# Kernel tuning notes

Hardware: AMD Instinct MI355X
Metric: run time of the kernel (lower is better)

The kernel has to match this reference:

```python
import jax, jax.numpy as jnp
import numpy as np

VOCAB = 512
EMB = 256
HID = 64
T_HORIZON = 0.05


def setup_inputs() -> dict:
    key = jax.random.key(0)
    ks = jax.random.split(key, 6)
    B, L = 32, 4096
    x = jax.random.randint(ks[0], (B, L), 0, VOCAB, dtype=jnp.int64 if jax.config.jax_enable_x64 else jnp.int32)
    emb_table = jax.random.normal(ks[1], (VOCAB, EMB), dtype=jnp.float32)
    W1 = jax.random.normal(ks[2], (EMB, HID), dtype=jnp.float32) * (1.0 / np.sqrt(EMB))
    b1 = jnp.zeros((HID,), dtype=jnp.float32)
    W2 = jax.random.normal(ks[3], (HID, VOCAB), dtype=jnp.float32) * (1.0 / np.sqrt(HID))
    b2 = jnp.full((VOCAB,), 0.1, dtype=jnp.float32)  # torch: bias.data.fill_(0.1)
    return {"x": x, "emb_table": emb_table, "W1": W1, "b1": b1, "W2": W2, "b2": b2, "steps": 5}


def reference(x, emb_table, W1, b1, W2, b2, steps):
    """Vectorized Gillespie-style Markov jump simulation.

    Equivalent to the torch loop: intensity is computed once per step from the
    current state, then every (b, l) position samples a candidate next state
    from softmax(intensity) with the self-transition zeroed and renormalized
    (== categorical over logits with the current state masked to -inf), and
    accepts it with prob 1 - exp(-rate * dt).
    """
    V = emb_table.shape[0]
    dt = T_HORIZON / steps
    key = jax.random.key(42)
    keys = jax.random.split(key, steps)
    vocab_ids = jnp.arange(V)

    def step(x_t, k):
        # intensity: [B, L, V]
        h = jax.nn.relu(emb_table[x_t] @ W1 + b1)
        intensity = h @ W2 + b2
        # mask self-transition (softmax * (1 - onehot) then renormalize)
        self_mask = x_t[..., None] == vocab_ids  # [B, L, V] bool
        masked_logits = jnp.where(self_mask, -jnp.inf, intensity)
        k1, k2 = jax.random.split(k)
        next_state = jax.random.categorical(k1, masked_logits)  # [B, L]
        rate = jnp.take_along_axis(intensity, next_state[..., None], axis=-1)[..., 0]
        accept_prob = 1.0 - jnp.exp(-rate * dt)
        u = jax.random.uniform(k2, x_t.shape, dtype=rate.dtype)
        x_t = jnp.where(u < accept_prob, next_state.astype(x_t.dtype), x_t)
        return x_t, None

    x_final, _ = jax.lax.scan(step, x, keys)
    return x_final
```

## Files before the change

kernel.cpp:

```cpp
#include <hip/hip_runtime.h>
#include <stdint.h>


#define VOCAB  512
#define EMB    256
#define HID    64
#define NPOS   (32 * 4096)
#define STEPS  5
#define JWAVES 8192

__host__ __device__ __forceinline__ void tf2x32(uint32_t k0, uint32_t k1,
                                                uint32_t x0, uint32_t x1,
                                                uint32_t& o0, uint32_t& o1) {
  uint32_t ks2 = k0 ^ k1 ^ 0x1BD11BDAu;
  x0 += k0; x1 += k1;
#define TFR(r) { x0 += x1; x1 = (x1 << (r)) | (x1 >> (32 - (r))); x1 ^= x0; }
  TFR(13) TFR(15) TFR(26) TFR(6)
  x0 += k1;  x1 += ks2 + 1u;
  TFR(17) TFR(29) TFR(16) TFR(24)
  x0 += ks2; x1 += k0 + 2u;
  TFR(13) TFR(15) TFR(26) TFR(6)
  x0 += k0;  x1 += k1 + 3u;
  TFR(17) TFR(29) TFR(16) TFR(24)
  x0 += k1;  x1 += ks2 + 4u;
  TFR(13) TFR(15) TFR(26) TFR(6)
  x0 += ks2; x1 += k0 + 5u;
#undef TFR
  o0 = x0; o1 = x1;
}

struct Keys {
  uint32_t k1a[STEPS], k1b[STEPS];
  uint32_t k2a[STEPS], k2b[STEPS];
};

__global__ __launch_bounds__(512)
void build_table(const float* __restrict__ emb,
                 const float* __restrict__ W1,
                 const float* __restrict__ b1,
                 const float* __restrict__ W2,
                 const float* __restrict__ b2,
                 float* __restrict__ I,
                 float* __restrict__ P,
                 float* __restrict__ pthr,
                 uint32_t* __restrict__ counter) {
  const int s   = blockIdx.x;
  const int tid = threadIdx.x;
  if (s == 0 && tid == 0) *counter = 0u;

  __shared__ double part[8][HID];
  __shared__ double hd[HID];
  __shared__ float  redmax[8];

  const int hid = tid & (HID - 1);
  const int kq  = tid >> 6;
  const float* e = emb + s * EMB;
  double acc = 0.0;
#pragma unroll
  for (int ib = 0; ib < 32; ib += 16) {
    float ev[16], wv[16];
#pragma unroll
    for (int i = 0; i < 16; ++i) {
      const int k = kq + 8 * (ib + i);
      ev[i] = e[k];
      wv[i] = W1[k * HID + hid];
    }
#pragma unroll
    for (int i = 0; i < 16; ++i)
      acc += (double)ev[i] * (double)wv[i];
  }
  part[kq][hid] = acc;
  __syncthreads();
  if (kq == 0) {
    const double a = ((part[0][hid] + part[1][hid]) + (part[2][hid] + part[3][hid]))
                   + ((part[4][hid] + part[5][hid]) + (part[6][hid] + part[7][hid]));
    const float m = (float)a + b1[hid];
    hd[hid] = (double)(m > 0.0f ? m : 0.0f);
  }
  __syncthreads();

  double acc2 = 0.0;
#pragma unroll
  for (int kb = 0; kb < HID; kb += 16) {
    float wv[16];
#pragma unroll
    for (int i = 0; i < 16; ++i)
      wv[i] = W2[(kb + i) * VOCAB + tid];
#pragma unroll
    for (int i = 0; i < 16; ++i)
      acc2 += hd[kb + i] * (double)wv[i];
  }
  const float val = (float)acc2 + b2[tid];
  I[s * VOCAB + tid] = val;
  const float z = (-val) * 0.01f;
  const float pv = 1.0f - (float)exp((double)z);
  P[s * VOCAB + tid] = pv;

  float lmax = pv;
  for (int off = 32; off > 0; off >>= 1)
    lmax = fmaxf(lmax, __shfl_xor(lmax, off, 64));
  if ((tid & 63) == 0) redmax[tid >> 6] = lmax;
  __syncthreads();
  if (tid == 0) {
    float m = redmax[0];
#pragma unroll
    for (int i = 1; i < 8; ++i) m = fmaxf(m, redmax[i]);
    pthr[s] = m;
  }
}

__global__ __launch_bounds__(256)
void screen_kernel(const int* __restrict__ x_in,
                   const float* __restrict__ pthr,
                   int* __restrict__ x_out,
                   uint32_t* __restrict__ counter,
                   uint32_t* __restrict__ list,
                   Keys K) {
  const int pos = blockIdx.x * 256 + threadIdx.x;
  const int s = x_in[pos];
  const float th = pthr[s];
  int mask = 0;
#pragma unroll
  for (int t = 0; t < STEPS; ++t) {
    uint32_t w0, w1;
    tf2x32(K.k2a[t], K.k2b[t], 0u, (uint32_t)pos, w0, w1);
    const float u = __uint_as_float((((w0 ^ w1) >> 9) | 0x3f800000u)) - 1.0f;
    if (u < th) mask |= (1 << t);
  }
  x_out[pos] = s;

  const int lane = threadIdx.x & 63, wv = threadIdx.x >> 6;
  const unsigned long long bal = __ballot(mask != 0);
  __shared__ uint32_t wcnt[4], wbase[4];
  if (lane == 0) wcnt[wv] = (uint32_t)__popcll(bal);
  __syncthreads();
  if (threadIdx.x == 0) {
    const uint32_t tot = wcnt[0] + wcnt[1] + wcnt[2] + wcnt[3];
    uint32_t b = atomicAdd(counter, tot);
    wbase[0] = b; b += wcnt[0];
    wbase[1] = b; b += wcnt[1];
    wbase[2] = b; b += wcnt[2];
    wbase[3] = b;
  }
  __syncthreads();
  if (mask) {
    const uint32_t off = wbase[wv] +
        (uint32_t)__popcll(bal & ((1ull << lane) - 1ull));
    list[off] = (uint32_t)pos | ((uint32_t)mask << 20);
  }
}

__global__ __launch_bounds__(128)
void jump_kernel(const int* __restrict__ x_in,
                 const float* __restrict__ I,
                 const float* __restrict__ P,
                 const float* __restrict__ pthr,
                 int* __restrict__ x_out,
                 const uint32_t* __restrict__ counter,
                 const uint32_t* __restrict__ list,
                 Keys K) {
  const int lane = threadIdx.x & 63;
  const int wid  = (blockIdx.x << 1) | (threadIdx.x >> 6);
  const int n = (int)*counter;
  const float TINYF = 1.17549435e-38f;
  const float NEGINF = -__builtin_inff();

  for (int i = wid; i < n; i += JWAVES) {
    const uint32_t e = list[i];
    const int pos = (int)(e & 0xFFFFFu);
    int m = (int)(e >> 20);
    int s = __builtin_amdgcn_readfirstlane(x_in[pos]);

    while (m) {
      const int t = __builtin_ctz(m);
      m &= m - 1;

      uint32_t a0, a1;
      tf2x32(K.k2a[t], K.k2b[t], 0u, (uint32_t)pos, a0, a1);
      const float u = __uint_as_float((((a0 ^ a1) >> 9) | 0x3f800000u)) - 1.0f;

      const float* row = I + s * VOCAB;
      float rv[8];
#pragma unroll
      for (int j = 0; j < 8; ++j)
        rv[j] = row[lane + (j << 6)];

      const uint32_t fbase = ((uint32_t)pos << 9) + (uint32_t)lane;
      uint32_t bits[8];
#pragma unroll
      for (int j = 0; j < 8; ++j) {
        uint32_t w0, w1;
        tf2x32(K.k1a[t], K.k1b[t], 0u, fbase + ((uint32_t)j << 6), w0, w1);
        bits[j] = w0 ^ w1;
      }

      float valC[8];
      float bestC = NEGINF;
#pragma unroll
      for (int j = 0; j < 8; ++j) {
        float ufv = __uint_as_float((bits[j] >> 9) | 0x3f800000u) - 1.0f;
        if (ufv == 0.0f) ufv = TINYF;
        const float gC = -__logf(-__logf(ufv));
        const int v = lane + (j << 6);
        valC[j] = (v == s) ? NEGINF : rv[j] + gC;
        bestC = fmaxf(bestC, valC[j]);
      }
      for (int off = 32; off > 0; off >>= 1)
        bestC = fmaxf(bestC, __shfl_xor(bestC, off, 64));
      const float thresh = bestC - 0.015625f;

      float best = NEGINF;
      int bidx = 0x7FFFFFFF;
#pragma unroll
      for (int j = 0; j < 8; ++j) {
        if (valC[j] >= thresh) {
          float ufv = __uint_as_float((bits[j] >> 9) | 0x3f800000u) - 1.0f;
          if (ufv == 0.0f) ufv = TINYF;
          const float g = -logf(-logf(ufv));
          const float val = rv[j] + g;
          const int v = lane + (j << 6);
          if (val > best) { best = val; bidx = v; }
        }
      }
      for (int off = 32; off > 0; off >>= 1) {
        const float ob = __shfl_xor(best, off, 64);
        const int   oi = __shfl_xor(bidx, off, 64);
        if (ob > best || (ob == best && oi < bidx)) { best = ob; bidx = oi; }
      }
      bidx = __builtin_amdgcn_readfirstlane(bidx);

      const float pacc = P[s * VOCAB + bidx];
      if (u < pacc) {
        s = bidx;
        const float th2 = pthr[s];
        int m2 = 0;
        for (int t2 = t + 1; t2 < STEPS; ++t2) {
          uint32_t w0, w1;
          tf2x32(K.k2a[t2], K.k2b[t2], 0u, (uint32_t)pos, w0, w1);
          const float u2 =
              __uint_as_float((((w0 ^ w1) >> 9) | 0x3f800000u)) - 1.0f;
          if (u2 < th2) m2 |= (1 << t2);
        }
        m = m2;
      }
    }
    if (lane == 0) x_out[pos] = s;
  }
}

extern "C" void kernel_launch(void* const* d_in, const int* in_sizes, int n_in,
                              void* d_out, int out_size, void* d_ws, size_t ws_size,
                              hipStream_t stream) {
  const int*   x   = (const int*)d_in[0];
  const float* emb = (const float*)d_in[1];
  const float* W1  = (const float*)d_in[2];
  const float* b1  = (const float*)d_in[3];
  const float* W2  = (const float*)d_in[4];
  const float* b2  = (const float*)d_in[5];
  float*    I       = (float*)d_ws;
  float*    P       = I + VOCAB * VOCAB;
  float*    pthr    = P + VOCAB * VOCAB;
  uint32_t* counter = (uint32_t*)(pthr + VOCAB);
  uint32_t* list    = counter + 32;
  int* out = (int*)d_out;

  Keys K;
  for (int t = 0; t < STEPS; ++t) {
    uint32_t Sa, Sb;
    tf2x32(0u, 42u, 0u, (uint32_t)t, Sa, Sb);
    tf2x32(Sa, Sb, 0u, 0u, K.k1a[t], K.k1b[t]);
    tf2x32(Sa, Sb, 0u, 1u, K.k2a[t], K.k2b[t]);
  }

  build_table<<<VOCAB, 512, 0, stream>>>(emb, W1, b1, W2, b2, I, P, pthr, counter);
  screen_kernel<<<NPOS / 256, 256, 0, stream>>>(x, pthr, out, counter, list, K);
  jump_kernel<<<JWAVES / 2, 128, 0, stream>>>(x, I, P, pthr, out, counter, list, K);
}
```

Baseline: 111.0 us.

## Process two candidate positions per wavefront using half-wave lanes

The jump kernel now splits each 64-lane wavefront into two 32-lane halves, each handling its own listed position across 16 vocab entries per lane, so twice as many positions are processed per wave. The current state is packed into the list entry, which removes the dependent x_in load, and the output is written only when the state changed. In exchange the two halves diverge because of __any loops, the RNG for rescreening is recomputed for all steps, and each lane holds more registers.

Measured after the change: 115.3 us. 1.04x slower.

```diff
diff --git a/kernel.cpp b/kernel.cpp
--- a/kernel.cpp
+++ b/kernel.cpp
@@ -146,13 +146,12 @@
   if (mask) {
     const uint32_t off = wbase[wv] +
         (uint32_t)__popcll(bal & ((1ull << lane) - 1ull));
-    list[off] = (uint32_t)pos | ((uint32_t)mask << 20);
+    list[off] = (uint32_t)pos | ((uint32_t)mask << 17) | ((uint32_t)s << 22);
   }
 }
 
 __global__ __launch_bounds__(128)
-void jump_kernel(const int* __restrict__ x_in,
-                 const float* __restrict__ I,
+void jump_kernel(const float* __restrict__ I,
                  const float* __restrict__ P,
                  const float* __restrict__ pthr,
                  int* __restrict__ x_out,
@@ -160,91 +159,102 @@
                  const uint32_t* __restrict__ list,
                  Keys K) {
   const int lane = threadIdx.x & 63;
-  const int wid  = (blockIdx.x << 1) | (threadIdx.x >> 6);
+  const int wid  = ((int)blockIdx.x << 1) | (threadIdx.x >> 6);
+  const int half = lane >> 5;
+  const int hl   = lane & 31;
   const int n = (int)*counter;
   const float TINYF = 1.17549435e-38f;
   const float NEGINF = -__builtin_inff();
-
-  for (int i = wid; i < n; i += JWAVES) {
-    const uint32_t e = list[i];
-    const int pos = (int)(e & 0xFFFFFu);
-    int m = (int)(e >> 20);
-    int s = __builtin_amdgcn_readfirstlane(x_in[pos]);
-
-    while (m) {
-      const int t = __builtin_ctz(m);
-      m &= m - 1;
+  const float MARGIN = 0.015625f;
+
+  for (int i0 = (wid << 1); i0 < n; i0 += (JWAVES << 1)) {
+    const int idx = i0 + half;
+    const bool alive = (idx < n);
+    const uint32_t e = alive ? list[idx] : 0u;
+    const int pos = (int)(e & 0x1FFFFu);
+    int m = (int)((e >> 17) & 0x1Fu);
+    int s = (int)(e >> 22);
+    bool changed = false;
+
+    while (__any(m != 0)) {
+      const bool act = (m != 0);
+      const int t = act ? __builtin_ctz((unsigned)m) : 0;
+      if (act) m &= m - 1;
 
       uint32_t a0, a1;
       tf2x32(K.k2a[t], K.k2b[t], 0u, (uint32_t)pos, a0, a1);
       const float u = __uint_as_float((((a0 ^ a1) >> 9) | 0x3f800000u)) - 1.0f;
 
       const float* row = I + s * VOCAB;
-      float rv[8];
-#pragma unroll
-      for (int j = 0; j < 8; ++j)
-        rv[j] = row[lane + (j << 6)];
-
-      const uint32_t fbase = ((uint32_t)pos << 9) + (uint32_t)lane;
-      uint32_t bits[8];
-#pragma unroll
-      for (int j = 0; j < 8; ++j) {
+      float rv[16];
+#pragma unroll
+      for (int j = 0; j < 16; ++j)
+        rv[j] = row[hl + (j << 5)];
+
+      const uint32_t fbase = ((uint32_t)pos << 9) + (uint32_t)hl;
+      uint32_t bits[16];
+#pragma unroll
+      for (int j = 0; j < 16; ++j) {
         uint32_t w0, w1;
-        tf2x32(K.k1a[t], K.k1b[t], 0u, fbase + ((uint32_t)j << 6), w0, w1);
+        tf2x32(K.k1a[t], K.k1b[t], 0u, fbase + ((uint32_t)j << 5), w0, w1);
         bits[j] = w0 ^ w1;
       }
 
-      float valC[8];
+      float valC[16];
       float bestC = NEGINF;
 #pragma unroll
-      for (int j = 0; j < 8; ++j) {
+      for (int j = 0; j < 16; ++j) {
         float ufv = __uint_as_float((bits[j] >> 9) | 0x3f800000u) - 1.0f;
         if (ufv == 0.0f) ufv = TINYF;
         const float gC = -__logf(-__logf(ufv));
-        const int v = lane + (j << 6);
+        const int v = hl + (j << 5);
         valC[j] = (v == s) ? NEGINF : rv[j] + gC;
         bestC = fmaxf(bestC, valC[j]);
       }
-      for (int off = 32; off > 0; off >>= 1)
+#pragma unroll
+      for (int off = 16; off > 0; off >>= 1)
         bestC = fmaxf(bestC, __shfl_xor(bestC, off, 64));
-      const float thresh = bestC - 0.015625f;
+      const float thresh = bestC - MARGIN;
 
       float best = NEGINF;
       int bidx = 0x7FFFFFFF;
 #pragma unroll
-      for (int j = 0; j < 8; ++j) {
+      for (int j = 0; j < 16; ++j) {
         if (valC[j] >= thresh) {
           float ufv = __uint_as_float((bits[j] >> 9) | 0x3f800000u) - 1.0f;
           if (ufv == 0.0f) ufv = TINYF;
           const float g = -logf(-logf(ufv));
           const float val = rv[j] + g;
-          const int v = lane + (j << 6);
+          const int v = hl + (j << 5);
           if (val > best) { best = val; bidx = v; }
         }
       }
-      for (int off = 32; off > 0; off >>= 1) {
+#pragma unroll
+      for (int off = 16; off > 0; off >>= 1) {
         const float ob = __shfl_xor(best, off, 64);
         const int   oi = __shfl_xor(bidx, off, 64);
         if (ob > best || (ob == best && oi < bidx)) { best = ob; bidx = oi; }
       }
-      bidx = __builtin_amdgcn_readfirstlane(bidx);
 
       const float pacc = P[s * VOCAB + bidx];
-      if (u < pacc) {
-        s = bidx;
-        const float th2 = pthr[s];
+      const bool accept = act && (u < pacc);
+      if (accept) { s = bidx; changed = true; }
+
+      if (__any(accept)) {
+        const float th2 = accept ? pthr[s] : 0.0f;
         int m2 = 0;
-        for (int t2 = t + 1; t2 < STEPS; ++t2) {
+#pragma unroll
+        for (int t2 = 1; t2 < STEPS; ++t2) {
           uint32_t w0, w1;
           tf2x32(K.k2a[t2], K.k2b[t2], 0u, (uint32_t)pos, w0, w1);
           const float u2 =
               __uint_as_float((((w0 ^ w1) >> 9) | 0x3f800000u)) - 1.0f;
-          if (u2 < th2) m2 |= (1 << t2);
+          if (t2 > t && u2 < th2) m2 |= (1 << t2);
         }
-        m = m2;
+        if (accept) m = m2;
       }
     }
-    if (lane == 0) x_out[pos] = s;
+    if (alive && changed && hl == 0) x_out[pos] = s;
   }
 }
 
@@ -274,5 +284,5 @@
 
   build_table<<<VOCAB, 512, 0, stream>>>(emb, W1, b1, W2, b2, I, P, pthr, counter);
   screen_kernel<<<NPOS / 256, 256, 0, stream>>>(x, pthr, out, counter, list, K);
-  jump_kernel<<<JWAVES / 2, 128, 0, stream>>>(x, I, P, pthr, out, counter, list, K);
-}
+  jump_kernel<<<JWAVES / 2, 128, 0, stream>>>(I, P, pthr, out, counter, list, K);
+}
```
